# Kernel tuning notes

Hardware: AMD Instinct MI355X
Metric: run time of the kernel (lower is better)

Reference implementation:

```python
import jax, jax.numpy as jnp
import numpy as np

N1, N2 = 8192, 8192
E1, E2 = 131072, 131072
F_IN, NH, B = 64, 128, 256
D6 = 6 * NH  # set2set in_channels = 768


def _gcn(x, W, b, src, dst, ew, n):
    xw = x @ W
    loop = jnp.arange(n)
    s = jnp.concatenate([src, loop])
    d = jnp.concatenate([dst, loop])
    w = jnp.concatenate([ew, jnp.ones((n,), ew.dtype)])
    deg = jax.ops.segment_sum(w, d, num_segments=n)
    dinv = jnp.where(deg > 0, jax.lax.rsqrt(deg), 0.0)
    norm = (dinv[s] * w * dinv[d])[:, None]
    return jax.ops.segment_sum(xw[s] * norm, d, num_segments=n) + b


def _leaky(x):
    return jax.nn.leaky_relu(x, 0.2)


def _l2norm(x):
    return x / jnp.maximum(jnp.linalg.norm(x, axis=1, keepdims=True), 1e-12)


def _set2set(x, batch, nseg, Wih, Whh, bih, bhh, steps=2):
    # Set2Set pooling: LSTM(input=2d, hidden=d) + segment softmax attention
    d = x.shape[1]
    h = jnp.zeros((nseg, d), x.dtype)
    c = jnp.zeros((nseg, d), x.dtype)
    q_star = jnp.zeros((nseg, 2 * d), x.dtype)
    for _ in range(steps):
        gates = q_star @ Wih.T + h @ Whh.T + bih + bhh
        gi, gf, gg, go = jnp.split(gates, 4, axis=1)  # torch LSTM gate order i,f,g,o
        c = jax.nn.sigmoid(gf) * c + jax.nn.sigmoid(gi) * jnp.tanh(gg)
        h = jax.nn.sigmoid(go) * jnp.tanh(c)
        e = jnp.sum(x * h[batch], axis=1)
        emax = jax.ops.segment_max(e, batch, num_segments=nseg)
        ee = jnp.exp(e - emax[batch])
        a = ee / jax.ops.segment_sum(ee, batch, num_segments=nseg)[batch]
        r = jax.ops.segment_sum(a[:, None] * x, batch, num_segments=nseg)
        q_star = jnp.concatenate([h, r], axis=1)
    return q_star


def setup_inputs():
    key = jax.random.key(0)
    ks = jax.random.split(key, 20)
    f32 = jnp.float32

    def xav(k, shp):
        fan_in, fan_out = shp[-1], shp[0] if len(shp) == 2 else shp[-1]
        lim = float(np.sqrt(6.0 / (shp[0] + shp[1])))
        return jax.random.uniform(k, shp, f32, -lim, lim)

    inp = {}
    inp["features_1"] = jax.random.normal(ks[0], (N1, F_IN), f32)
    inp["features_2"] = jax.random.normal(ks[1], (N2, F_IN), f32)
    inp["edge_attr_1"] = jax.random.uniform(ks[2], (E1,), f32)
    inp["edge_attr_2"] = jax.random.uniform(ks[3], (E2,), f32)
    inp["W0"] = xav(ks[4], (F_IN, NH)); inp["b0"] = jnp.zeros((NH,), f32)
    inp["W1"] = xav(ks[5], (NH, NH)); inp["b1"] = jnp.zeros((NH,), f32)
    inp["W2"] = xav(ks[6], (NH, NH)); inp["b2"] = jnp.zeros((NH,), f32)
    inp["Wih"] = xav(ks[7], (4 * D6, 2 * D6)); inp["bih"] = jnp.zeros((4 * D6,), f32)
    inp["Whh"] = xav(ks[8], (4 * D6, D6)); inp["bhh"] = jnp.zeros((4 * D6,), f32)
    inp["Wp1"] = xav(ks[9], (256, 4 * D6)); inp["bp1"] = jnp.zeros((256,), f32)
    inp["Wp2"] = xav(ks[10], (128, 256)); inp["bp2"] = jnp.zeros((128,), f32)
    inp["Wp3"] = xav(ks[11], (1, 128)); inp["bp3"] = jnp.zeros((1,), f32)
    inp["edge_index_1"] = jax.random.randint(ks[12], (2, E1), 0, N1)
    inp["edge_index_2"] = jax.random.randint(ks[13], (2, E2), 0, N2)
    inp["batch_1"] = jnp.sort(jax.random.randint(ks[14], (N1,), 0, B))
    inp["batch_2"] = jnp.sort(jax.random.randint(ks[15], (N2,), 0, B))
    return inp


def reference(features_1, features_2, edge_attr_1, edge_attr_2,
              W0, b0, W1, b1, W2, b2, Wih, bih, Whh, bhh,
              Wp1, bp1, Wp2, bp2, Wp3, bp3,
              edge_index_1, edge_index_2, batch_1, batch_2):
    s1, d1 = edge_index_1[0], edge_index_1[1]
    s2, d2 = edge_index_2[0], edge_index_2[1]

    f1a = _leaky(_gcn(features_1, W0, b0, s1, d1, edge_attr_1, N1))
    f2a = _leaky(_gcn(features_2, W0, b0, s2, d2, edge_attr_2, N2))
    f1b = _leaky(_gcn(f1a, W1, b1, s1, d1, edge_attr_1, N1))
    f2b = _leaky(_gcn(f2a, W1, b1, s2, d2, edge_attr_2, N2))
    f1c = _leaky(_gcn(f1b, W2, b2, s1, d1, edge_attr_1, N1))
    f2c = _leaky(_gcn(f2b, W2, b2, s2, d2, edge_attr_2, N2))
    h1 = jnp.concatenate([f1a, f1b, f1c], axis=1)  # [N1, 3*NH]
    h2 = jnp.concatenate([f2a, f2b, f2c], axis=1)  # [N2, 3*NH]

    # interaction: cosine-sim map masked to same-graph pairs (len_map)
    ns = _l2norm(h1)
    nv = _l2norm(h2)
    mask = (batch_1[:, None] == batch_2[None, :]).astype(ns.dtype)  # [N1, N2]
    imap = (ns @ nv.T) * mask
    f1 = jnp.concatenate([ns, imap @ nv], axis=1)      # [N1, 6*NH]
    f2 = jnp.concatenate([nv, imap.T @ ns], axis=1)    # [N2, 6*NH]

    g1 = _set2set(f1, batch_1, B, Wih, Whh, bih, bhh)  # [B, 12*NH]
    g2 = _set2set(f2, batch_2, B, Wih, Whh, bih, bhh)  # [B, 12*NH]
    z = jnp.concatenate([g1, g2], axis=1)              # [B, 24*NH]
    z = jax.nn.relu(z @ Wp1.T + bp1)
    z = jax.nn.relu(z @ Wp2.T + bp2)
    z = z @ Wp3.T + bp3
    return jax.nn.sigmoid(z).reshape(-1)
```

## Files before the change

### kernel.cpp

```cpp
#include <hip/hip_runtime.h>
#include <cmath>

#define N_NODES 8192
#define N_EDGES 131072
#define NB      256
#define NH      128
#define D3      384
#define D6      768
#define SMM     96

typedef __attribute__((ext_vector_type(8))) short short8v;
typedef __attribute__((ext_vector_type(4))) float f32x4;
typedef unsigned short bf16t;

__device__ __forceinline__ float sigf(float x){ return 1.0f/(1.0f+__expf(-x)); }
__device__ __forceinline__ unsigned short f2bf(float x){
  unsigned u = __float_as_uint(x);
  unsigned r = u + 0x7FFF + ((u>>16)&1);
  return (unsigned short)(r>>16);
}
__device__ __forceinline__ float bfl(unsigned u){ return __uint_as_float(u<<16); }
__device__ __forceinline__ float bfh(unsigned u){ return __uint_as_float(u & 0xFFFF0000u); }
__device__ __forceinline__ float b2f(bf16t u){ return __uint_as_float(((unsigned)u)<<16); }


__global__ void k_init(float* deg1, float* deg2, int* ecnt1, int* ecnt2, int* cnt1, int* cnt2){
  int t = blockIdx.x*blockDim.x + threadIdx.x;
  if (t < N_NODES){ deg1[t]=1.f; deg2[t]=1.f; ecnt1[t]=0; ecnt2[t]=0; }
  if (t < NB){ cnt1[t]=0; cnt2[t]=0; }
}

__global__ void k_deg(const int* __restrict__ ei1, const float* __restrict__ ea1, float* deg1, int* ecnt1,
                      const int* __restrict__ ei2, const float* __restrict__ ea2, float* deg2, int* ecnt2,
                      const int* __restrict__ b1, const int* __restrict__ b2, int* cnt1, int* cnt2){
  int idx = blockIdx.x*blockDim.x + threadIdx.x;
  int side = idx >= N_EDGES;
  int e = idx & (N_EDGES-1);
  const int* ei = side? ei2:ei1; const float* ea = side? ea2:ea1;
  float* deg = side? deg2:deg1;  int* ecnt = side? ecnt2:ecnt1;
  int d = ei[N_EDGES+e];
  atomicAdd(&deg[d], ea[e]);
  atomicAdd(&ecnt[d], 1);
  if (idx < N_NODES){ atomicAdd(&cnt1[b1[idx]],1); atomicAdd(&cnt2[b2[idx]],1); }
}

__global__ void k_dinv(float* deg1, float* deg2){
  int t = blockIdx.x*blockDim.x + threadIdx.x;
  if (t < N_NODES){ deg1[t]=rsqrtf(deg1[t]); deg2[t]=rsqrtf(deg2[t]); }
}

__global__ __launch_bounds__(256) void k_scan256(const int* c1, const int* c2, int* s1, int* s2){
  const int* c = blockIdx.x? c2:c1; int* st = blockIdx.x? s2:s1;
  __shared__ int ps[256];
  int t = threadIdx.x;
  ps[t]=c[t]; __syncthreads();
  for (int d=1; d<256; d<<=1){
    int v = (t>=d)? ps[t-d]:0;
    __syncthreads();
    ps[t]+=v;
    __syncthreads();
  }
  st[t+1]=ps[t];
  if (t==0) st[0]=0;
}

__global__ __launch_bounds__(1024) void k_escan(const int* ec1, const int* ec2,
                                                int* off1, int* cur1, int* off2, int* cur2){
  const int* cnt = blockIdx.x? ec2:ec1;
  int* off = blockIdx.x? off2:off1;
  int* cur = blockIdx.x? cur2:cur1;
  __shared__ int ps[1024];
  int t = threadIdx.x;
  int base = t*8;
  int loc[8]; int s=0;
  #pragma unroll
  for (int k=0;k<8;k++){ loc[k]=s; s+=cnt[base+k]; }
  ps[t]=s; __syncthreads();
  for (int d=1; d<1024; d<<=1){
    int v = (t>=d)? ps[t-d]:0;
    __syncthreads();
    ps[t]+=v;
    __syncthreads();
  }
  int pre = (t==0)? 0 : ps[t-1];
  #pragma unroll
  for (int k=0;k<8;k++){ int v=pre+loc[k]; off[base+k]=v; cur[base+k]=v; }
  if (t==1023) off[N_NODES]=ps[1023];
}

__global__ void k_fill(const int* __restrict__ ei1, const float* __restrict__ ea1, const float* __restrict__ d1,
                       int* cur1, int* es1, float* ec1,
                       const int* __restrict__ ei2, const float* __restrict__ ea2, const float* __restrict__ d2,
                       int* cur2, int* es2, float* ec2){
  int idx = blockIdx.x*blockDim.x + threadIdx.x;
  int side = idx >= N_EDGES;
  int e = idx & (N_EDGES-1);
  const int* ei = side? ei2:ei1; const float* ea = side? ea2:ea1;
  const float* dinv = side? d2:d1;
  int* cur = side? cur2:cur1; int* es = side? es2:es1; float* ec = side? ec2:ec1;
  int s = ei[e], d = ei[N_EDGES+e];
  int pos = atomicAdd(&cur[d], 1);
  es[pos] = s;
  ec[pos] = dinv[s]*ea[e]*dinv[d];
}

__global__ __launch_bounds__(256) void k_szero(uint4* p){
  p[blockIdx.x*256 + threadIdx.x] = make_uint4(0,0,0,0);
}


__global__ __launch_bounds__(128) void k_xw(const float* __restrict__ x1, const float* __restrict__ x2,
                                            int xs, int K, const float* __restrict__ W,
                                            bf16t* __restrict__ xw1, bf16t* __restrict__ xw2){
  __shared__ float xr[8][128];
  int blk = blockIdx.x;
  int side = blk >> 10; int b = blk & 1023;
  const float* x = side? x2:x1;
  bf16t* xw = side? xw2:xw1;
  int i0 = b*8;
  int c = threadIdx.x;
  for (int idx=c; idx<8*K; idx+=128){
    int r = idx / K, k = idx - r*K;
    xr[r][k] = x[(size_t)(i0+r)*xs + k];
  }
  __syncthreads();
  float acc[8]={0,0,0,0,0,0,0,0};
  for (int k=0;k<K;k++){
    float w = W[k*NH+c];
    #pragma unroll
    for (int r=0;r<8;r++) acc[r]+=xr[r][k]*w;
  }
  #pragma unroll
  for (int r=0;r<8;r++) xw[(size_t)(i0+r)*NH+c]=f2bf(acc[r]);
}

__global__ __launch_bounds__(256) void k_gather(const bf16t* __restrict__ xw1, const bf16t* __restrict__ xw2,
                                                const int* __restrict__ off1, const int* __restrict__ off2,
                                                const int* __restrict__ es1, const int* __restrict__ es2,
                                                const float* __restrict__ ec1, const float* __restrict__ ec2,
                                                const float* __restrict__ d1, const float* __restrict__ d2,
                                                const float* __restrict__ b,
                                                float* __restrict__ h1, float* __restrict__ h2, int loff){
  int blk = blockIdx.x;
  int side = blk >> 10; int bb = blk & 1023;
  const ushort4* xw = (const ushort4*)(side? xw2:xw1);
  const int* off = side? off2:off1;
  const int* es  = side? es2:es1;
  const float* ec= side? ec2:ec1;
  const float* dinv = side? d2:d1;
  float* h = side? h2:h1;
  int t = threadIdx.x;
  int i = bb*8 + (t>>5);
  int c4 = t & 31;
  float dv = dinv[i];
  ushort4 v = xw[(size_t)i*32 + c4];
  float sc = dv*dv;
  float4 acc = {b2f(v.x)*sc, b2f(v.y)*sc, b2f(v.z)*sc, b2f(v.w)*sc};
  int r = off[i], r1 = off[i+1];
  for (; r+3<r1; r+=4){
    int s0=es[r], s1=es[r+1], s2=es[r+2], s3=es[r+3];
    float w0=ec[r], w1=ec[r+1], w2=ec[r+2], w3=ec[r+3];
    ushort4 u0 = xw[(size_t)s0*32 + c4];
    ushort4 u1 = xw[(size_t)s1*32 + c4];
    ushort4 u2 = xw[(size_t)s2*32 + c4];
    ushort4 u3 = xw[(size_t)s3*32 + c4];
    acc.x += b2f(u0.x)*w0 + b2f(u1.x)*w1 + b2f(u2.x)*w2 + b2f(u3.x)*w3;
    acc.y += b2f(u0.y)*w0 + b2f(u1.y)*w1 + b2f(u2.y)*w2 + b2f(u3.y)*w3;
    acc.z += b2f(u0.z)*w0 + b2f(u1.z)*w1 + b2f(u2.z)*w2 + b2f(u3.z)*w3;
    acc.w += b2f(u0.w)*w0 + b2f(u1.w)*w1 + b2f(u2.w)*w2 + b2f(u3.w)*w3;
  }
  for (; r<r1; r++){
    int s0=es[r]; float w0=ec[r];
    ushort4 u0 = xw[(size_t)s0*32 + c4];
    acc.x+=b2f(u0.x)*w0; acc.y+=b2f(u0.y)*w0; acc.z+=b2f(u0.z)*w0; acc.w+=b2f(u0.w)*w0;
  }
  float4 bv = ((const float4*)b)[c4];
  acc.x+=bv.x; acc.y+=bv.y; acc.z+=bv.z; acc.w+=bv.w;
  acc.x = (acc.x>0.f)?acc.x:0.2f*acc.x;
  acc.y = (acc.y>0.f)?acc.y:0.2f*acc.y;
  acc.z = (acc.z>0.f)?acc.z:0.2f*acc.z;
  acc.w = (acc.w>0.f)?acc.w:0.2f*acc.w;
  ((float4*)(h + (size_t)i*D3 + loff))[c4] = acc;
}

__global__ __launch_bounds__(128) void k_l2norm(const float* __restrict__ h1, const float* __restrict__ h2,
                                                bf16t* __restrict__ f1, bf16t* __restrict__ f2){
  int blk = blockIdx.x;
  int side = blk >> 13; int i = blk & (N_NODES-1);
  const float* h = side? h2:h1; bf16t* f = side? f2:f1;
  int t = threadIdx.x;
  float v0=h[(size_t)i*D3+t], v1=h[(size_t)i*D3+128+t], v2=h[(size_t)i*D3+256+t];
  float ss = v0*v0+v1*v1+v2*v2;
  #pragma unroll
  for (int o=32;o;o>>=1) ss += __shfl_down(ss,o,64);
  __shared__ float ws[2];
  if ((t&63)==0) ws[t>>6]=ss;
  __syncthreads();
  float scale = 1.0f/fmaxf(sqrtf(ws[0]+ws[1]), 1e-12f);
  f[(size_t)i*D6+t]      = f2bf(v0*scale);
  f[(size_t)i*D6+128+t]  = f2bf(v1*scale);
  f[(size_t)i*D6+256+t]  = f2bf(v2*scale);
}

__global__ __launch_bounds__(256) void k_smat(const bf16t* __restrict__ f1, const bf16t* __restrict__ f2,
                                              const int* __restrict__ st1, const int* __restrict__ st2,
                                              bf16t* __restrict__ S, bf16t* __restrict__ ST){
  int g = blockIdx.x;
  int it2 = blockIdx.y/3, jt2 = blockIdx.y - it2*3;
  int i0 = st1[g]; int n1 = st1[g+1]-i0; if (n1>SMM) n1=SMM;
  int j0 = st2[g]; int n2 = st2[g+1]-j0; if (n2>SMM) n2=SMM;
  if (it2*32 >= n1 || jt2*32 >= n2) return;
  int w = threadIdx.x >> 6, lane = threadIdx.x & 63;
  int lm = lane & 15, quad = lane >> 4;
  int ti = it2*2 + (w>>1), tj = jt2*2 + (w&1);
  if (ti*16 >= n1 || tj*16 >= n2) return;
  const bf16t* a = f1 + (size_t)(i0 + ti*16 + lm)*D6 + quad*8;
  const bf16t* b = f2 + (size_t)(j0 + tj*16 + lm)*D6 + quad*8;
  f32x4 acc = {0,0,0,0};
  #pragma unroll
  for (int k=0; k<384; k+=32){
    short8v af = *(const short8v*)(a + k);
    short8v bf = *(const short8v*)(b + k);
    acc = __builtin_amdgcn_mfma_f32_16x16x32_bf16(af, bf, acc, 0, 0, 0);
  }
  bf16t* Sg  = S  + (size_t)g*SMM*SMM;
  bf16t* STg = ST + (size_t)g*SMM*SMM;
  int col = tj*16 + lm;
  #pragma unroll
  for (int r=0;r<4;r++){
    int row = ti*16 + quad*4 + r;
    if (row < n1 && col < n2){
      bf16t v = f2bf(acc[r]);
      Sg [(size_t)row*SMM + col] = v;
      STg[(size_t)col*SMM + row] = v;
    }
  }
}

__global__ __launch_bounds__(256) void k_apply(bf16t* __restrict__ f1, bf16t* __restrict__ f2,
                                               const int* __restrict__ st1, const int* __restrict__ st2,
                                               const bf16t* __restrict__ S, const bf16t* __restrict__ ST){
  __shared__ bf16t tbuf[32*392];
  int bx = blockIdx.x;
  int side = bx >> 8, g = bx & (NB-1);
  int a0 = st1[g]; int n1 = st1[g+1]-a0; if (n1>SMM) n1=SMM;
  int b0 = st2[g]; int n2 = st2[g+1]-b0; if (n2>SMM) n2=SMM;
  int cnt = side? n2 : n1;
  int J   = side? n1 : n2;
  int r0 = blockIdx.y*32;
  if (r0 >= cnt) return;
  const bf16t* src = side? (f1 + (size_t)a0*D6) : (f2 + (size_t)b0*D6);
  bf16t* dst = (side? (f2 + (size_t)b0*D6) : (f1 + (size_t)a0*D6)) + D3;
  const bf16t* Sg = (side? ST : S) + (size_t)g*SMM*SMM;
  int t = threadIdx.x, w = t>>6, lane = t&63;
  int lm = lane & 15, quad = lane >> 4;
  int mt1 = (cnt - r0 > 16) ? 2 : 1;
  f32x4 acc[2][6] = {};
  for (int kb = 0; kb < J; kb += 32){
    __syncthreads();
    for (int idx = t; idx < 32*48; idx += 256){
      int j = idx/48, cg = idx - j*48;
      uint4 v = (kb+j < J)? ((const uint4*)(src + (size_t)(kb+j)*D6))[cg] : make_uint4(0,0,0,0);
      *(uint4*)(tbuf + j*392 + cg*8) = v;
    }
    short8v af0, af1;
    {
      const bf16t* ap = Sg + (size_t)(r0 + lm)*SMM + kb + quad*8;
      af0 = *(const short8v*)ap;
      af1 = (mt1 > 1)? *(const short8v*)(ap + 16*SMM) : af0;
    }
    __syncthreads();
    #pragma unroll
    for (int ni = 0; ni < 6; ni++){
      int nt = w*6 + ni;
      short8v bf;
      #pragma unroll
      for (int ji = 0; ji < 8; ji++)
        bf[ji] = (short)tbuf[(quad*8 + ji)*392 + nt*16 + lm];
      acc[0][ni] = __builtin_amdgcn_mfma_f32_16x16x32_bf16(af0, bf, acc[0][ni], 0, 0, 0);
      if (mt1 > 1)
        acc[1][ni] = __builtin_amdgcn_mfma_f32_16x16x32_bf16(af1, bf, acc[1][ni], 0, 0, 0);
    }
  }
  for (int mt = 0; mt < mt1; mt++)
    for (int ni = 0; ni < 6; ni++){
      int nt = w*6 + ni;
      #pragma unroll
      for (int r = 0; r < 4; r++){
        int row = r0 + mt*16 + quad*4 + r;
        if (row < cnt) dst[(size_t)row*D6 + nt*16 + lm] = f2bf(acc[mt][ni][r]);
      }
    }
}


__global__ void k_h0(const float* bih, const float* bhh, float* h0, float* c0){
  int j = threadIdx.x;
  float gi = bih[j]      + bhh[j];
  float gg = bih[2*D6+j] + bhh[2*D6+j];
  float go = bih[3*D6+j] + bhh[3*D6+j];
  float c = sigf(gi)*tanhf(gg);
  c0[j]=c;
  h0[j]=sigf(go)*tanhf(c);
}

__global__ __launch_bounds__(64) void k_cvec(const float* __restrict__ Wih, const float* __restrict__ Whh,
                                             const float* bih, const float* bhh,
                                             const float* __restrict__ h0, float* __restrict__ cvec){
  int j = blockIdx.x, lane = threadIdx.x;
  const float4* wi = (const float4*)(Wih + (size_t)j*(2*D6));
  const float4* wh = (const float4*)(Whh + (size_t)j*D6);
  const float4* h4 = (const float4*)h0;
  float acc=0;
  #pragma unroll
  for (int m=0;m<3;m++){
    float4 hv = h4[m*64+lane];
    float4 a = wi[m*64+lane];
    float4 b = wh[m*64+lane];
    acc += hv.x*(a.x+b.x) + hv.y*(a.y+b.y) + hv.z*(a.z+b.z) + hv.w*(a.w+b.w);
  }
  #pragma unroll
  for (int m=1;m<64;m<<=1) acc += __shfl_xor(acc,m,64);
  if (lane==0) cvec[j]=acc+bih[j]+bhh[j];
}

__global__ __launch_bounds__(256) void k_att(const bf16t* __restrict__ f1, const bf16t* __restrict__ f2,
                                             const float* __restrict__ hbase, int perseg,
                                             const int* __restrict__ st1, const int* __restrict__ st2,
                                             bf16t* __restrict__ dst16, long sidestep, long dstride){
  __shared__ float4 hs[192];
  __shared__ float e_s[SMM];
  int side = blockIdx.x >> 8, g = blockIdx.x & (NB-1);
  const int* st = side? st2:st1;
  int n0 = st[g]; int cnt = st[g+1]-n0; if (cnt>SMM) cnt=SMM;
  const bf16t* x = (side? f2:f1) + (size_t)n0*D6;
  const float* hv = hbase + (perseg? (size_t)(side*NB+g)*D6 : 0);
  int t = threadIdx.x, w = t>>6, lane = t&63;
  if (t<192) hs[t] = ((const float4*)hv)[t];
  __syncthreads();
  for (int n=w; n<cnt; n+=4){
    const uint2* xr = (const uint2*)(x + (size_t)n*D6);
    float p = 0;
    #pragma unroll
    for (int m=0;m<3;m++){
      uint2 rv = xr[m*64+lane];
      float4 hvv = hs[m*64+lane];
      p += bfl(rv.x)*hvv.x + bfh(rv.x)*hvv.y + bfl(rv.y)*hvv.z + bfh(rv.y)*hvv.w;
    }
    #pragma unroll
    for (int m=1;m<64;m<<=1) p += __shfl_xor(p,m,64);
    if (lane==0) e_s[n]=p;
  }
  __syncthreads();
  if (w==0){
    float mx=-INFINITY;
    for (int n=lane;n<cnt;n+=64) mx=fmaxf(mx,e_s[n]);
    #pragma unroll
    for (int m=1;m<64;m<<=1) mx=fmaxf(mx,__shfl_xor(mx,m,64));
    float s=0;
    for (int n=lane;n<cnt;n+=64) s+=__expf(e_s[n]-mx);
    #pragma unroll
    for (int m=1;m<64;m<<=1) s+=__shfl_xor(s,m,64);
    float inv=1.0f/s;
    for (int n=lane;n<cnt;n+=64) e_s[n]=__expf(e_s[n]-mx)*inv;
  }
  __syncthreads();
  if (t<192){
    float4 acc={0,0,0,0};
    for (int n=0;n<cnt;n++){
      float a = e_s[n];
      uint2 rv = ((const uint2*)(x + (size_t)n*D6))[t];
      acc.x+=a*bfl(rv.x); acc.y+=a*bfh(rv.x); acc.z+=a*bfl(rv.y); acc.w+=a*bfh(rv.y);
    }
    ushort4 o = make_ushort4(f2bf(acc.x), f2bf(acc.y), f2bf(acc.z), f2bf(acc.w));
    ((ushort4*)(dst16 + side*sidestep + (size_t)g*dstride))[t]=o;
  }
}

__global__ __launch_bounds__(256) void k_gemm_mfma(const short* __restrict__ A16,
                                                   const short* __restrict__ B16,
                                                   float* __restrict__ pout){
  int w = threadIdx.x >> 6, lane = threadIdx.x & 63;
  int lm = lane & 15, quad = lane >> 4;
  int bm = blockIdx.x * 16;
  int bn = blockIdx.y * 256 + w * 64;
  const short* a = A16 + (size_t)(bm + lm)*768 + quad*8;
  const short* b = B16 + (size_t)(bn + lm)*768 + quad*8;
  f32x4 acc0={0,0,0,0}, acc1={0,0,0,0}, acc2={0,0,0,0}, acc3={0,0,0,0};
  for (int k=0; k<768; k+=32){
    short8v af = *(const short8v*)(a + k);
    short8v b0 = *(const short8v*)(b + k);
    short8v b1 = *(const short8v*)(b + 16*768 + k);
    short8v b2 = *(const short8v*)(b + 32*768 + k);
    short8v b3 = *(const short8v*)(b + 48*768 + k);
    acc0 = __builtin_amdgcn_mfma_f32_16x16x32_bf16(af, b0, acc0, 0, 0, 0);
    acc1 = __builtin_amdgcn_mfma_f32_16x16x32_bf16(af, b1, acc1, 0, 0, 0);
    acc2 = __builtin_amdgcn_mfma_f32_16x16x32_bf16(af, b2, acc2, 0, 0, 0);
    acc3 = __builtin_amdgcn_mfma_f32_16x16x32_bf16(af, b3, acc3, 0, 0, 0);
  }
  #pragma unroll
  for (int r=0;r<4;r++){
    size_t base = (size_t)(bm + quad*4 + r)*3072 + bn + lm;
    pout[base]      = acc0[r];
    pout[base + 16] = acc1[r];
    pout[base + 32] = acc2[r];
    pout[base + 48] = acc3[r];
  }
}

__global__ __launch_bounds__(256) void k_gemm_mfma_p1(const short* __restrict__ A16,
                                                      const short* __restrict__ B16,
                                                      float* __restrict__ pout){
  int w = threadIdx.x >> 6, lane = threadIdx.x & 63;
  int lm = lane & 15, quad = lane >> 4;
  int bm = blockIdx.x * 16;
  int bn = w * 64;
  int kbase = blockIdx.y * 192;
  const short* a = A16 + (size_t)(bm + lm)*3072 + quad*8 + kbase;
  const short* b = B16 + (size_t)(bn + lm)*3072 + quad*8 + kbase;
  f32x4 acc0={0,0,0,0}, acc1={0,0,0,0}, acc2={0,0,0,0}, acc3={0,0,0,0};
  for (int k=0; k<192; k+=32){
    short8v af = *(const short8v*)(a + k);
    short8v b0 = *(const short8v*)(b + k);
    short8v b1 = *(const short8v*)(b + 16*3072 + k);
    short8v b2 = *(const short8v*)(b + 32*3072 + k);
    short8v b3 = *(const short8v*)(b + 48*3072 + k);
    acc0 = __builtin_amdgcn_mfma_f32_16x16x32_bf16(af, b0, acc0, 0, 0, 0);
    acc1 = __builtin_amdgcn_mfma_f32_16x16x32_bf16(af, b1, acc1, 0, 0, 0);
    acc2 = __builtin_amdgcn_mfma_f32_16x16x32_bf16(af, b2, acc2, 0, 0, 0);
    acc3 = __builtin_amdgcn_mfma_f32_16x16x32_bf16(af, b3, acc3, 0, 0, 0);
  }
  float* po = pout + (size_t)blockIdx.y*256*256;
  #pragma unroll
  for (int r=0;r<4;r++){
    size_t base = (size_t)(bm + quad*4 + r)*256 + bn + lm;
    po[base]      = acc0[r];
    po[base + 16] = acc1[r];
    po[base + 32] = acc2[r];
    po[base + 48] = acc3[r];
  }
}

__global__ __launch_bounds__(256) void k_conv_w(const float* __restrict__ W, short* __restrict__ dst){
  int t = blockIdx.x*256 + threadIdx.x;
  int n = t/192, q = t - n*192;
  float4 v = ((const float4*)(W + (size_t)n*1536 + 768))[q];
  short4 o = { (short)f2bf(v.x), (short)f2bf(v.y), (short)f2bf(v.z), (short)f2bf(v.w) };
  ((short4*)dst)[t] = o;
}

__global__ __launch_bounds__(256) void k_conv(const float* __restrict__ src, short* __restrict__ dst){
  int t = blockIdx.x*256 + threadIdx.x;
  float4 v = ((const float4*)src)[t];
  short4 o = { (short)f2bf(v.x), (short)f2bf(v.y), (short)f2bf(v.z), (short)f2bf(v.w) };
  ((short4*)dst)[t] = o;
}

__global__ __launch_bounds__(256) void k_reduce(const float* __restrict__ partial, int S, long MN,
                                                const float* __restrict__ cv, float* __restrict__ dst,
                                                int N, int act){
  long idx = (long)blockIdx.x*256 + threadIdx.x;
  if (idx >= MN) return;
  float s = 0;
  for (int p=0;p<S;p++) s += partial[(size_t)p*MN + idx];
  s += cv[idx % N];
  if (act) s = fmaxf(s,0.f);
  dst[idx]=s;
}

__global__ __launch_bounds__(256) void k_lstm_red(const float* __restrict__ pbuf,
                                                  const float* __restrict__ cvec,
                                                  const float* __restrict__ c0,
                                                  float* __restrict__ h1s, bf16t* __restrict__ z16){
  int t = blockIdx.x*256 + threadIdx.x;
  int m = t/D6, j = t - m*D6;
  const float* p0 = pbuf + (size_t)m*3072 + j;
  float g4[4];
  #pragma unroll
  for (int q=0;q<4;q++) g4[q] = cvec[q*D6 + j] + p0[q*D6];
  float c = sigf(g4[1])*c0[j] + sigf(g4[0])*tanhf(g4[2]);
  float h = sigf(g4[3])*tanhf(c);
  h1s[(size_t)m*D6 + j] = h;
  int side = m>>8, g = m&255;
  z16[(size_t)g*3072 + side*1536 + j] = f2bf(h);
}

__global__ __launch_bounds__(128) void k_p23(const float* __restrict__ z1,
                                             const float* __restrict__ Wp2, const float* __restrict__ bp2,
                                             const float* __restrict__ Wp3, const float* __restrict__ bp3,
                                             float* __restrict__ out){
  __shared__ float zr[256];
  __shared__ float ws[2];
  int m = blockIdx.x, t = threadIdx.x;
  ((float2*)zr)[t] = ((const float2*)(z1 + m*256))[t];
  __syncthreads();
  const float4* wrow = (const float4*)(Wp2 + (size_t)t*256);
  const float4* z4 = (const float4*)zr;
  float acc = bp2[t];
  #pragma unroll 8
  for (int k=0;k<64;k++){
    float4 wv = wrow[k], zv = z4[k];
    acc += wv.x*zv.x + wv.y*zv.y + wv.z*zv.z + wv.w*zv.w;
  }
  float p = fmaxf(acc,0.f)*Wp3[t];
  #pragma unroll
  for (int o=32;o;o>>=1) p += __shfl_down(p,o,64);
  if ((t&63)==0) ws[t>>6]=p;
  __syncthreads();
  if (t==0){ float v=ws[0]+ws[1]+bp3[0]; out[m]=1.0f/(1.0f+__expf(-v)); }
}


extern "C" void kernel_launch(void* const* d_in, const int* in_sizes, int n_in,
                              void* d_out, int out_size, void* d_ws, size_t ws_size,
                              hipStream_t stream){
  const float* feat1=(const float*)d_in[0];
  const float* feat2=(const float*)d_in[1];
  const float* ea1  =(const float*)d_in[2];
  const float* ea2  =(const float*)d_in[3];
  const float* W0=(const float*)d_in[4];  const float* b0=(const float*)d_in[5];
  const float* W1=(const float*)d_in[6];  const float* b1=(const float*)d_in[7];
  const float* W2=(const float*)d_in[8];  const float* b2=(const float*)d_in[9];
  const float* Wih=(const float*)d_in[10]; const float* bih=(const float*)d_in[11];
  const float* Whh=(const float*)d_in[12]; const float* bhh=(const float*)d_in[13];
  const float* Wp1=(const float*)d_in[14]; const float* bp1=(const float*)d_in[15];
  const float* Wp2=(const float*)d_in[16]; const float* bp2=(const float*)d_in[17];
  const float* Wp3=(const float*)d_in[18]; const float* bp3=(const float*)d_in[19];
  const int* ei1=(const int*)d_in[20]; const int* ei2=(const int*)d_in[21];
  const int* batch1=(const int*)d_in[22]; const int* batch2=(const int*)d_in[23];
  float* out = (float*)d_out;

  float* base = (float*)d_ws;
  size_t off = 0;
  auto alloc = [&](size_t n)->float* { float* r = base + off; off += (n + 255) & ~(size_t)255; return r; };
  float* deg1 = alloc(N_NODES);          float* deg2 = alloc(N_NODES);
  bf16t* xw1  = (bf16t*)alloc((size_t)N_NODES*NH/2);
  bf16t* xw2  = (bf16t*)alloc((size_t)N_NODES*NH/2);
  float* h1   = alloc((size_t)N_NODES*D3);
  float* h2   = alloc((size_t)N_NODES*D3);
  bf16t* f1   = (bf16t*)alloc((size_t)N_NODES*D6/2);
  bf16t* f2   = (bf16t*)alloc((size_t)N_NODES*D6/2);
  float* ecoef1 = alloc(N_EDGES);        float* ecoef2 = alloc(N_EDGES);
  float* h0   = alloc(D6);  float* c0 = alloc(D6);  float* cvec = alloc(4*D6);
  bf16t* Sbuf = (bf16t*)alloc((size_t)NB*SMM*SMM);
  bf16t* STbuf= Sbuf + (size_t)NB*SMM*SMM;
  float* h1s  = alloc((size_t)512*D6);
  bf16t* zbuf16 = (bf16t*)alloc((size_t)256*3072/2);
  float* z1   = alloc((size_t)256*256);
  float* pbuf = alloc((size_t)4*512*3072);
  short* Abuf16 = (short*)alloc((size_t)512*D6/2);
  short* Wih16  = (short*)alloc((size_t)3072*D6/2);
  short* Wp116  = (short*)alloc((size_t)256*3072/2);
  int* cnt1 = (int*)alloc(NB);   int* cnt2 = (int*)alloc(NB);
  int* st1  = (int*)alloc(NB+1); int* st2  = (int*)alloc(NB+1);
  int* ecnt1= (int*)alloc(N_NODES); int* ecnt2 = (int*)alloc(N_NODES);
  int* eoff1= (int*)alloc(N_NODES+1); int* eoff2 = (int*)alloc(N_NODES+1);
  int* ecur1= (int*)alloc(N_NODES); int* ecur2 = (int*)alloc(N_NODES);
  int* esrc1= (int*)alloc(N_EDGES); int* esrc2 = (int*)alloc(N_EDGES);
  (void)ws_size; (void)in_sizes; (void)n_in; (void)out_size;

  k_init   <<<32,256,0,stream>>>(deg1,deg2,ecnt1,ecnt2,cnt1,cnt2);
  k_deg    <<<1024,256,0,stream>>>(ei1,ea1,deg1,ecnt1, ei2,ea2,deg2,ecnt2, batch1,batch2,cnt1,cnt2);
  k_dinv   <<<32,256,0,stream>>>(deg1,deg2);
  k_scan256<<<2,256,0,stream>>>(cnt1,cnt2,st1,st2);
  k_escan  <<<2,1024,0,stream>>>(ecnt1,ecnt2,eoff1,ecur1,eoff2,ecur2);
  k_fill   <<<1024,256,0,stream>>>(ei1,ea1,deg1,ecur1,esrc1,ecoef1, ei2,ea2,deg2,ecur2,esrc2,ecoef2);
  k_conv_w <<<2304,256,0,stream>>>(Wih, Wih16);
  k_conv   <<<768,256,0,stream>>>(Wp1, Wp116);
  k_szero  <<<2304,256,0,stream>>>((uint4*)Sbuf);

  const float* Ws[3]={W0,W1,W2}; const float* bs[3]={b0,b1,b2};
  for (int l=0;l<3;l++){
    const float* x1 = (l==0)? feat1 : (h1 + (l-1)*NH);
    const float* x2 = (l==0)? feat2 : (h2 + (l-1)*NH);
    int xs = (l==0)? 64 : D3;
    int K  = (l==0)? 64 : NH;
    k_xw    <<<2048,128,0,stream>>>(x1,x2,xs,K,Ws[l],xw1,xw2);
    k_gather<<<2048,256,0,stream>>>(xw1,xw2,eoff1,eoff2,esrc1,esrc2,ecoef1,ecoef2,
                                    deg1,deg2,bs[l],h1,h2,l*NH);
  }

  k_l2norm<<<16384,128,0,stream>>>(h1,h2,f1,f2);
  k_smat  <<<dim3(256,9),256,0,stream>>>(f1,f2,st1,st2,Sbuf,STbuf);
  k_apply <<<dim3(512,3),256,0,stream>>>(f1,f2,st1,st2,Sbuf,STbuf);

  k_h0  <<<1,768,0,stream>>>(bih,bhh,h0,c0);
  k_cvec<<<3072,64,0,stream>>>(Wih,Whh,bih,bhh,h0,cvec);

  k_att<<<512,256,0,stream>>>(f1,f2,h0,0,st1,st2,(bf16t*)Abuf16,(long)256*D6,(long)D6);

  k_gemm_mfma<<<dim3(32,12),256,0,stream>>>(Abuf16, Wih16, pbuf);
  k_lstm_red <<<1536,256,0,stream>>>(pbuf,cvec,c0,h1s,zbuf16);

  k_att<<<512,256,0,stream>>>(f1,f2,h1s,1,st1,st2,zbuf16+768,(long)1536,(long)3072);

  k_gemm_mfma_p1<<<dim3(16,16),256,0,stream>>>((const short*)zbuf16, Wp116, pbuf);
  k_reduce <<<256,256,0,stream>>>(pbuf,16,(long)256*256, bp1, z1, 256, 1);
  k_p23 <<<256,128,0,stream>>>(z1, Wp2, bp2, Wp3, bp3, out);
}
```

Measured before the change: 394.0 us.

## Fuse small kernels: dinv, l2norm, h0, reduce into neighbors; parallelize attention readout

Removes four launches by folding the degree rsqrt into edge fill and gather, the L2 normalisation into the last GCN gather layer, the LSTM initial-state computation into its consumers, and the partial-sum reduction into the final MLP kernel. The attention readout now splits nodes across all four waves with a shared-memory partial reduction instead of a serial loop over nodes in 192 threads. The aim is to cut launch overhead and intermediate global traffic. In exchange, h0 is recomputed redundantly in many blocks and extra shared memory is used in k_att.

```diff
diff --git a/kernel.cpp b/kernel.cpp
--- a/kernel.cpp
+++ b/kernel.cpp
@@ -22,6 +22,10 @@
 __device__ __forceinline__ float bfl(unsigned u){ return __uint_as_float(u<<16); }
 __device__ __forceinline__ float bfh(unsigned u){ return __uint_as_float(u & 0xFFFF0000u); }
 __device__ __forceinline__ float b2f(bf16t u){ return __uint_as_float(((unsigned)u)<<16); }
+__device__ __forceinline__ float h0val(const float* bih, const float* bhh, int j){
+  float c = sigf(bih[j]+bhh[j]) * tanhf(bih[2*D6+j]+bhh[2*D6+j]);
+  return sigf(bih[3*D6+j]+bhh[3*D6+j]) * tanhf(c);
+}
 
 
 __global__ void k_init(float* deg1, float* deg2, int* ecnt1, int* ecnt2, int* cnt1, int* cnt2){
@@ -44,11 +48,6 @@
   if (idx < N_NODES){ atomicAdd(&cnt1[b1[idx]],1); atomicAdd(&cnt2[b2[idx]],1); }
 }
 
-__global__ void k_dinv(float* deg1, float* deg2){
-  int t = blockIdx.x*blockDim.x + threadIdx.x;
-  if (t < N_NODES){ deg1[t]=rsqrtf(deg1[t]); deg2[t]=rsqrtf(deg2[t]); }
-}
-
 __global__ __launch_bounds__(256) void k_scan256(const int* c1, const int* c2, int* s1, int* s2){
   const int* c = blockIdx.x? c2:c1; int* st = blockIdx.x? s2:s1;
   __shared__ int ps[256];
@@ -96,12 +95,12 @@
   int side = idx >= N_EDGES;
   int e = idx & (N_EDGES-1);
   const int* ei = side? ei2:ei1; const float* ea = side? ea2:ea1;
-  const float* dinv = side? d2:d1;
+  const float* deg = side? d2:d1;
   int* cur = side? cur2:cur1; int* es = side? es2:es1; float* ec = side? ec2:ec1;
   int s = ei[e], d = ei[N_EDGES+e];
   int pos = atomicAdd(&cur[d], 1);
   es[pos] = s;
-  ec[pos] = dinv[s]*ea[e]*dinv[d];
+  ec[pos] = rsqrtf(deg[s])*ea[e]*rsqrtf(deg[d]);
 }
 
 __global__ __launch_bounds__(256) void k_szero(uint4* p){
@@ -140,21 +139,21 @@
                                                 const float* __restrict__ ec1, const float* __restrict__ ec2,
                                                 const float* __restrict__ d1, const float* __restrict__ d2,
                                                 const float* __restrict__ b,
-                                                float* __restrict__ h1, float* __restrict__ h2, int loff){
+                                                float* __restrict__ h1, float* __restrict__ h2, int loff,
+                                                int l2mode, bf16t* __restrict__ f1, bf16t* __restrict__ f2){
   int blk = blockIdx.x;
   int side = blk >> 10; int bb = blk & 1023;
   const ushort4* xw = (const ushort4*)(side? xw2:xw1);
   const int* off = side? off2:off1;
   const int* es  = side? es2:es1;
   const float* ec= side? ec2:ec1;
-  const float* dinv = side? d2:d1;
+  const float* deg = side? d2:d1;
   float* h = side? h2:h1;
   int t = threadIdx.x;
   int i = bb*8 + (t>>5);
   int c4 = t & 31;
-  float dv = dinv[i];
+  float sc = 1.0f/deg[i];
   ushort4 v = xw[(size_t)i*32 + c4];
-  float sc = dv*dv;
   float4 acc = {b2f(v.x)*sc, b2f(v.y)*sc, b2f(v.z)*sc, b2f(v.w)*sc};
   int r = off[i], r1 = off[i+1];
   for (; r+3<r1; r+=4){
@@ -180,26 +179,22 @@
   acc.y = (acc.y>0.f)?acc.y:0.2f*acc.y;
   acc.z = (acc.z>0.f)?acc.z:0.2f*acc.z;
   acc.w = (acc.w>0.f)?acc.w:0.2f*acc.w;
-  ((float4*)(h + (size_t)i*D3 + loff))[c4] = acc;
-}
-
-__global__ __launch_bounds__(128) void k_l2norm(const float* __restrict__ h1, const float* __restrict__ h2,
-                                                bf16t* __restrict__ f1, bf16t* __restrict__ f2){
-  int blk = blockIdx.x;
-  int side = blk >> 13; int i = blk & (N_NODES-1);
-  const float* h = side? h2:h1; bf16t* f = side? f2:f1;
-  int t = threadIdx.x;
-  float v0=h[(size_t)i*D3+t], v1=h[(size_t)i*D3+128+t], v2=h[(size_t)i*D3+256+t];
-  float ss = v0*v0+v1*v1+v2*v2;
-  #pragma unroll
-  for (int o=32;o;o>>=1) ss += __shfl_down(ss,o,64);
-  __shared__ float ws[2];
-  if ((t&63)==0) ws[t>>6]=ss;
-  __syncthreads();
-  float scale = 1.0f/fmaxf(sqrtf(ws[0]+ws[1]), 1e-12f);
-  f[(size_t)i*D6+t]      = f2bf(v0*scale);
-  f[(size_t)i*D6+128+t]  = f2bf(v1*scale);
-  f[(size_t)i*D6+256+t]  = f2bf(v2*scale);
+  if (!l2mode){
+    ((float4*)(h + (size_t)i*D3 + loff))[c4] = acc;
+  } else {
+    float4 v0 = ((const float4*)(h + (size_t)i*D3))[c4];
+    float4 v1 = ((const float4*)(h + (size_t)i*D3 + 128))[c4];
+    float ss = v0.x*v0.x+v0.y*v0.y+v0.z*v0.z+v0.w*v0.w
+             + v1.x*v1.x+v1.y*v1.y+v1.z*v1.z+v1.w*v1.w
+             + acc.x*acc.x+acc.y*acc.y+acc.z*acc.z+acc.w*acc.w;
+    #pragma unroll
+    for (int m=1;m<32;m<<=1) ss += __shfl_xor(ss, m, 64);
+    float scale = 1.0f/fmaxf(sqrtf(ss), 1e-12f);
+    bf16t* f = side? f2:f1;
+    ((ushort4*)(f + (size_t)i*D6))[c4]       = make_ushort4(f2bf(v0.x*scale),f2bf(v0.y*scale),f2bf(v0.z*scale),f2bf(v0.w*scale));
+    ((ushort4*)(f + (size_t)i*D6 + 128))[c4] = make_ushort4(f2bf(v1.x*scale),f2bf(v1.y*scale),f2bf(v1.z*scale),f2bf(v1.w*scale));
+    ((ushort4*)(f + (size_t)i*D6 + 256))[c4] = make_ushort4(f2bf(acc.x*scale),f2bf(acc.y*scale),f2bf(acc.z*scale),f2bf(acc.w*scale));
+  }
 }
 
 __global__ __launch_bounds__(256) void k_smat(const bf16t* __restrict__ f1, const bf16t* __restrict__ f2,
@@ -294,23 +289,16 @@
 }
 
 
-__global__ void k_h0(const float* bih, const float* bhh, float* h0, float* c0){
-  int j = threadIdx.x;
-  float gi = bih[j]      + bhh[j];
-  float gg = bih[2*D6+j] + bhh[2*D6+j];
-  float go = bih[3*D6+j] + bhh[3*D6+j];
-  float c = sigf(gi)*tanhf(gg);
-  c0[j]=c;
-  h0[j]=sigf(go)*tanhf(c);
-}
-
 __global__ __launch_bounds__(64) void k_cvec(const float* __restrict__ Wih, const float* __restrict__ Whh,
-                                             const float* bih, const float* bhh,
-                                             const float* __restrict__ h0, float* __restrict__ cvec){
+                                             const float* __restrict__ bih, const float* __restrict__ bhh,
+                                             float* __restrict__ cvec){
+  __shared__ float hs[D6];
   int j = blockIdx.x, lane = threadIdx.x;
+  for (int k=lane; k<D6; k+=64) hs[k] = h0val(bih,bhh,k);
+  __syncthreads();
   const float4* wi = (const float4*)(Wih + (size_t)j*(2*D6));
   const float4* wh = (const float4*)(Whh + (size_t)j*D6);
-  const float4* h4 = (const float4*)h0;
+  const float4* h4 = (const float4*)hs;
   float acc=0;
   #pragma unroll
   for (int m=0;m<3;m++){
@@ -326,17 +314,25 @@
 
 __global__ __launch_bounds__(256) void k_att(const bf16t* __restrict__ f1, const bf16t* __restrict__ f2,
                                              const float* __restrict__ hbase, int perseg,
+                                             const float* __restrict__ bih, const float* __restrict__ bhh,
                                              const int* __restrict__ st1, const int* __restrict__ st2,
                                              bf16t* __restrict__ dst16, long sidestep, long dstride){
   __shared__ float4 hs[192];
   __shared__ float e_s[SMM];
+  __shared__ float part[4][D6];
   int side = blockIdx.x >> 8, g = blockIdx.x & (NB-1);
   const int* st = side? st2:st1;
   int n0 = st[g]; int cnt = st[g+1]-n0; if (cnt>SMM) cnt=SMM;
   const bf16t* x = (side? f2:f1) + (size_t)n0*D6;
-  const float* hv = hbase + (perseg? (size_t)(side*NB+g)*D6 : 0);
   int t = threadIdx.x, w = t>>6, lane = t&63;
-  if (t<192) hs[t] = ((const float4*)hv)[t];
+  if (t<192){
+    if (perseg){
+      hs[t] = ((const float4*)(hbase + (size_t)(side*NB+g)*D6))[t];
+    } else {
+      int j = t*4;
+      hs[t] = make_float4(h0val(bih,bhh,j), h0val(bih,bhh,j+1), h0val(bih,bhh,j+2), h0val(bih,bhh,j+3));
+    }
+  }
   __syncthreads();
   for (int n=w; n<cnt; n+=4){
     const uint2* xr = (const uint2*)(x + (size_t)n*D6);
@@ -365,14 +361,28 @@
     for (int n=lane;n<cnt;n+=64) e_s[n]=__expf(e_s[n]-mx)*inv;
   }
   __syncthreads();
+  float av[3][4] = {};
+  for (int n=w; n<cnt; n+=4){
+    float a = e_s[n];
+    const uint2* xr = (const uint2*)(x + (size_t)n*D6);
+    #pragma unroll
+    for (int m=0;m<3;m++){
+      uint2 rv = xr[m*64+lane];
+      av[m][0]+=a*bfl(rv.x); av[m][1]+=a*bfh(rv.x); av[m][2]+=a*bfl(rv.y); av[m][3]+=a*bfh(rv.y);
+    }
+  }
+  #pragma unroll
+  for (int m=0;m<3;m++)
+    *(float4*)&part[w][(m*64+lane)*4] = make_float4(av[m][0],av[m][1],av[m][2],av[m][3]);
+  __syncthreads();
   if (t<192){
-    float4 acc={0,0,0,0};
-    for (int n=0;n<cnt;n++){
-      float a = e_s[n];
-      uint2 rv = ((const uint2*)(x + (size_t)n*D6))[t];
-      acc.x+=a*bfl(rv.x); acc.y+=a*bfh(rv.x); acc.z+=a*bfl(rv.y); acc.w+=a*bfh(rv.y);
-    }
-    ushort4 o = make_ushort4(f2bf(acc.x), f2bf(acc.y), f2bf(acc.z), f2bf(acc.w));
+    float4 p0 = *(const float4*)&part[0][t*4];
+    float4 p1 = *(const float4*)&part[1][t*4];
+    float4 p2 = *(const float4*)&part[2][t*4];
+    float4 p3 = *(const float4*)&part[3][t*4];
+    float4 s = make_float4(p0.x+p1.x+p2.x+p3.x, p0.y+p1.y+p2.y+p3.y,
+                           p0.z+p1.z+p2.z+p3.z, p0.w+p1.w+p2.w+p3.w);
+    ushort4 o = make_ushort4(f2bf(s.x), f2bf(s.y), f2bf(s.z), f2bf(s.w));
     ((ushort4*)(dst16 + side*sidestep + (size_t)g*dstride))[t]=o;
   }
 }
@@ -456,21 +466,9 @@
   ((short4*)dst)[t] = o;
 }
 
-__global__ __launch_bounds__(256) void k_reduce(const float* __restrict__ partial, int S, long MN,
-                                                const float* __restrict__ cv, float* __restrict__ dst,
-                                                int N, int act){
-  long idx = (long)blockIdx.x*256 + threadIdx.x;
-  if (idx >= MN) return;
-  float s = 0;
-  for (int p=0;p<S;p++) s += partial[(size_t)p*MN + idx];
-  s += cv[idx % N];
-  if (act) s = fmaxf(s,0.f);
-  dst[idx]=s;
-}
-
 __global__ __launch_bounds__(256) void k_lstm_red(const float* __restrict__ pbuf,
                                                   const float* __restrict__ cvec,
-                                                  const float* __restrict__ c0,
+                                                  const float* __restrict__ bih, const float* __restrict__ bhh,
                                                   float* __restrict__ h1s, bf16t* __restrict__ z16){
   int t = blockIdx.x*256 + threadIdx.x;
   int m = t/D6, j = t - m*D6;
@@ -478,21 +476,29 @@
   float g4[4];
   #pragma unroll
   for (int q=0;q<4;q++) g4[q] = cvec[q*D6 + j] + p0[q*D6];
-  float c = sigf(g4[1])*c0[j] + sigf(g4[0])*tanhf(g4[2]);
+  float c0j = sigf(bih[j]+bhh[j]) * tanhf(bih[2*D6+j]+bhh[2*D6+j]);
+  float c = sigf(g4[1])*c0j + sigf(g4[0])*tanhf(g4[2]);
   float h = sigf(g4[3])*tanhf(c);
   h1s[(size_t)m*D6 + j] = h;
   int side = m>>8, g = m&255;
   z16[(size_t)g*3072 + side*1536 + j] = f2bf(h);
 }
 
-__global__ __launch_bounds__(128) void k_p23(const float* __restrict__ z1,
+__global__ __launch_bounds__(128) void k_p23(const float* __restrict__ pbuf, const float* __restrict__ bp1,
                                              const float* __restrict__ Wp2, const float* __restrict__ bp2,
                                              const float* __restrict__ Wp3, const float* __restrict__ bp3,
                                              float* __restrict__ out){
   __shared__ float zr[256];
   __shared__ float ws[2];
   int m = blockIdx.x, t = threadIdx.x;
-  ((float2*)zr)[t] = ((const float2*)(z1 + m*256))[t];
+  float2 zacc = ((const float2*)(bp1))[t];
+  #pragma unroll
+  for (int p=0;p<16;p++){
+    float2 v = ((const float2*)(pbuf + (size_t)p*256*256 + (size_t)m*256))[t];
+    zacc.x += v.x; zacc.y += v.y;
+  }
+  zr[2*t]   = fmaxf(zacc.x, 0.f);
+  zr[2*t+1] = fmaxf(zacc.y, 0.f);
   __syncthreads();
   const float4* wrow = (const float4*)(Wp2 + (size_t)t*256);
   const float4* z4 = (const float4*)zr;
@@ -541,12 +547,11 @@
   bf16t* f1   = (bf16t*)alloc((size_t)N_NODES*D6/2);
   bf16t* f2   = (bf16t*)alloc((size_t)N_NODES*D6/2);
   float* ecoef1 = alloc(N_EDGES);        float* ecoef2 = alloc(N_EDGES);
-  float* h0   = alloc(D6);  float* c0 = alloc(D6);  float* cvec = alloc(4*D6);
+  float* cvec = alloc(4*D6);
   bf16t* Sbuf = (bf16t*)alloc((size_t)NB*SMM*SMM);
   bf16t* STbuf= Sbuf + (size_t)NB*SMM*SMM;
   float* h1s  = alloc((size_t)512*D6);
   bf16t* zbuf16 = (bf16t*)alloc((size_t)256*3072/2);
-  float* z1   = alloc((size_t)256*256);
   float* pbuf = alloc((size_t)4*512*3072);
   short* Abuf16 = (short*)alloc((size_t)512*D6/2);
   short* Wih16  = (short*)alloc((size_t)3072*D6/2);
@@ -561,7 +566,6 @@
 
   k_init   <<<32,256,0,stream>>>(deg1,deg2,ecnt1,ecnt2,cnt1,cnt2);
   k_deg    <<<1024,256,0,stream>>>(ei1,ea1,deg1,ecnt1, ei2,ea2,deg2,ecnt2, batch1,batch2,cnt1,cnt2);
-  k_dinv   <<<32,256,0,stream>>>(deg1,deg2);
   k_scan256<<<2,256,0,stream>>>(cnt1,cnt2,st1,st2);
   k_escan  <<<2,1024,0,stream>>>(ecnt1,ecnt2,eoff1,ecur1,eoff2,ecur2);
   k_fill   <<<1024,256,0,stream>>>(ei1,ea1,deg1,ecur1,esrc1,ecoef1, ei2,ea2,deg2,ecur2,esrc2,ecoef2);
@@ -577,24 +581,23 @@
     int K  = (l==0)? 64 : NH;
     k_xw    <<<2048,128,0,stream>>>(x1,x2,xs,K,Ws[l],xw1,xw2);
     k_gather<<<2048,256,0,stream>>>(xw1,xw2,eoff1,eoff2,esrc1,esrc2,ecoef1,ecoef2,
-                                    deg1,deg2,bs[l],h1,h2,l*NH);
-  }
-
-  k_l2norm<<<16384,128,0,stream>>>(h1,h2,f1,f2);
+                                    deg1,deg2,bs[l],h1,h2,l*NH,(l==2)?1:0,f1,f2);
+  }
+
   k_smat  <<<dim3(256,9),256,0,stream>>>(f1,f2,st1,st2,Sbuf,STbuf);
   k_apply <<<dim3(512,3),256,0,stream>>>(f1,f2,st1,st2,Sbuf,STbuf);
 
-  k_h0  <<<1,768,0,stream>>>(bih,bhh,h0,c0);
-  k_cvec<<<3072,64,0,stream>>>(Wih,Whh,bih,bhh,h0,cvec);
-
-  k_att<<<512,256,0,stream>>>(f1,f2,h0,0,st1,st2,(bf16t*)Abuf16,(long)256*D6,(long)D6);
+  k_cvec<<<3072,64,0,stream>>>(Wih,Whh,bih,bhh,cvec);
+
+  k_att<<<512,256,0,stream>>>(f1,f2,(const float*)nullptr,0,bih,bhh,st1,st2,
+                              (bf16t*)Abuf16,(long)256*D6,(long)D6);
 
   k_gemm_mfma<<<dim3(32,12),256,0,stream>>>(Abuf16, Wih16, pbuf);
-  k_lstm_red <<<1536,256,0,stream>>>(pbuf,cvec,c0,h1s,zbuf16);
-
-  k_att<<<512,256,0,stream>>>(f1,f2,h1s,1,st1,st2,zbuf16+768,(long)1536,(long)3072);
+  k_lstm_red <<<1536,256,0,stream>>>(pbuf,cvec,bih,bhh,h1s,zbuf16);
+
+  k_att<<<512,256,0,stream>>>(f1,f2,h1s,1,bih,bhh,st1,st2,
+                              zbuf16+768,(long)1536,(long)3072);
 
   k_gemm_mfma_p1<<<dim3(16,16),256,0,stream>>>((const short*)zbuf16, Wp116, pbuf);
-  k_reduce <<<256,256,0,stream>>>(pbuf,16,(long)256*256, bp1, z1, 256, 1);
-  k_p23 <<<256,128,0,stream>>>(z1, Wp2, bp2, Wp3, bp3, out);
-}
+  k_p23 <<<256,128,0,stream>>>(pbuf, bp1, Wp2, bp2, Wp3, bp3, out);
+}
```

Measured after the change: 389.0 us. Within noise of the previous version (-1.3%).
